# Kernel tuning notes

Measured on AMD Instinct MI355X. Metric: run time of the kernel, lower is better.

Reference implementation:

```python
import jax, jax.numpy as jnp
import numpy as np

S, N, H, AD, AR = 256, 1024, 512, 128, 2

def setup_inputs() -> dict:
    key = jax.random.key(0)
    k0, k1, k2, k3, k4, k5 = jax.random.split(key, 6)
    xav1 = np.sqrt(2.0 / (H + AD)).astype(np.float32)   # xavier_normal std for [H,AD]
    xav2 = np.sqrt(2.0 / (AD + AR)).astype(np.float32)  # xavier_normal std for [AD,AR]
    return {
        "pre_emb_padded": jax.random.normal(k0, (S, N, H), jnp.float32),
        "fol_emb_padded": jax.random.normal(k1, (S, N, H), jnp.float32),
        "pre_attn_mask": jnp.zeros((N, S), jnp.bool_),
        "fol_attn_mask": jnp.zeros((N, S), jnp.bool_),
        "pre_is_valid": jnp.ones((N,), jnp.int32),
        "fol_is_valid": jnp.ones((N,), jnp.int32),
        "W1_pre": jax.random.normal(k2, (H, AD), jnp.float32) * xav1,
        "W2_pre": jax.random.normal(k3, (AD, AR), jnp.float32) * xav2,
        "W1_fol": jax.random.normal(k4, (H, AD), jnp.float32) * xav1,
        "W2_fol": jax.random.normal(k5, (AD, AR), jnp.float32) * xav2,
    }

def _attn_pool(emb, mask, W1, W2):
    # emb: [S, N, H] -> x: [N, S, H]
    x = jnp.transpose(emb, (1, 0, 2))
    s = jnp.tanh(x @ W1) @ W2                 # [N, S, 2]
    s = jax.nn.softmax(s, axis=1)             # softmax over seq (first softmax)
    s = jnp.transpose(s, (0, 2, 1))           # [N, 2, S]
    s = jnp.where(mask[:, None, :], -jnp.inf, s)
    s = jax.nn.softmax(s, axis=-1)            # masked second softmax over seq
    return jnp.einsum('nrs,nsh->nrh', s, x)   # [N, 2, H]

def _scatter_valid(h, valid):
    # reproduce the python valid-list gather: valid rows take next chunk, else zeros
    pos = jnp.cumsum(valid) - 1               # [N]
    return jnp.where((valid > 0)[:, None, None], h[pos], jnp.zeros((), h.dtype))

def reference(pre_emb_padded, fol_emb_padded, pre_attn_mask, fol_attn_mask,
              pre_is_valid, fol_is_valid, W1_pre, W2_pre, W1_fol, W2_fol):
    h_pre = _scatter_valid(_attn_pool(pre_emb_padded, pre_attn_mask, W1_pre, W2_pre), pre_is_valid)
    h_fol = _scatter_valid(_attn_pool(fol_emb_padded, fol_attn_mask, W1_fol, W2_fol), fol_is_valid)
    # mean over the attn_r=2 rows, concat along feature dim -> [N, 1, 2H]
    return jnp.concatenate([h_pre.mean(axis=1, keepdims=True),
                            h_fol.mean(axis=1, keepdims=True)], axis=2)
```

## Files before the change

kernel.cpp:

```cpp
#include <hip/hip_runtime.h>
#include <hip/hip_bf16.h>
#include <cstdint>
#include <cstddef>

#define S_ 256
#define N_ 1024
#define H_ 512
#define AD_ 128
static constexpr int M_TOTAL = N_ * S_;

typedef __attribute__((ext_vector_type(8))) short short8;
typedef __attribute__((ext_vector_type(4))) float f32x4;

#define LDS_BARRIER()                                       \
  asm volatile("s_waitcnt lgkmcnt(0)" ::: "memory");        \
  __builtin_amdgcn_s_barrier()

__device__ __forceinline__ float red16_dpp(float v) {
  union fi { float f; int i; };
  fi a, r;
  a.f = v;
  r.i = __builtin_amdgcn_update_dpp(0, a.i, 0xB1, 0xF, 0xF, true);
  a.f += r.f;
  r.i = __builtin_amdgcn_update_dpp(0, a.i, 0x4E, 0xF, 0xF, true);
  a.f += r.f;
  r.i = __builtin_amdgcn_update_dpp(0, a.i, 0x124, 0xF, 0xF, true);
  a.f += r.f;
  r.i = __builtin_amdgcn_update_dpp(0, a.i, 0x128, 0xF, 0xF, true);
  a.f += r.f;
  return a.f;
}

__global__ __launch_bounds__(256) void k_w1frag(
    const float* __restrict__ w1_pre, const float* __restrict__ w1_fol,
    unsigned short* __restrict__ w1f) {
  int idx = blockIdx.x * 256 + threadIdx.x;
  int st = blockIdx.y;
  const float* w1 = st ? w1_fol : w1_pre;
  int j = idx & 7;
  int lane = (idx >> 3) & 63;
  int c = (idx >> 9) & 7;
  int kk = idx >> 12;
  int k = kk * 32 + ((lane >> 4) << 3) + j;
  int d = c * 16 + (lane & 15);
  __hip_bfloat16 hb = __float2bfloat16(w1[(size_t)k * AD_ + d]);
  w1f[(size_t)st * 65536 + idx] = *(unsigned short*)&hb;
}

__global__ __launch_bounds__(1024) void k_scan(
    const int* __restrict__ valid_pre, const int* __restrict__ valid_fol,
    int* __restrict__ pos) {
  const int st = blockIdx.x;
  const int* valid = st ? valid_fol : valid_pre;
  __shared__ int buf[1024];
  const int t = threadIdx.x;
  buf[t] = valid[t];
  __syncthreads();
  for (int off = 1; off < 1024; off <<= 1) {
    int v = (t >= off) ? buf[t - off] : 0;
    __syncthreads();
    buf[t] += v;
    __syncthreads();
  }
  pos[st * N_ + t] = buf[t] - 1;
}

__global__ __launch_bounds__(512) void k_logits(
    const float* __restrict__ emb_pre, const float* __restrict__ emb_fol,
    const unsigned short* __restrict__ w1f,
    const float* __restrict__ w2_pre, const float* __restrict__ w2_fol,
    float* __restrict__ logits) {
  __shared__ __align__(16) unsigned char As[32768];
  __shared__ float part[2][8][16][2];

  const int bid = blockIdx.x;
  const int st  = bid >> 7;
  const int idx = bid & 127;
  const int nc  = idx >> 1;
  const int sh  = idx & 1;
  const int n0 = nc * 16, s0 = sh * 128;
  const float* __restrict__ emb = st ? emb_fol : emb_pre;
  const float* __restrict__ w2  = st ? w2_fol : w2_pre;

  const int t = threadIdx.x;
  const int w = t >> 6, lane = t & 63;
  const int r16 = lane & 15, kq = lane >> 4;

  short8 B[16];
  {
    const unsigned short* bb = w1f + (size_t)st * 65536 + w * 512 + (size_t)lane * 8;
#pragma unroll
    for (int kk = 0; kk < 16; ++kk) B[kk] = *(const short8*)(bb + kk * 4096);
  }
  const float w2v0 = w2[(w * 16 + r16) * 2 + 0];
  const float w2v1 = w2[(w * 16 + r16) * 2 + 1];

  const int srow = t >> 5;
  const int sl   = t & 31;
  const size_t SSTR = (size_t)N_ * H_;
  const float* sbase = emb + ((size_t)s0 * N_ + n0 + srow) * H_ + sl * 4;
  unsigned wadr[4];
#pragma unroll
  for (int j = 0; j < 4; ++j) {
    int g = j * 16 + (sl >> 1);
    wadr[j] = (unsigned)(srow * 1024 + ((g ^ (srow & 7)) * 16) + (sl & 1) * 8);
  }
  const int rrow = w * 2 + ((lane >> 1) & 1);
  const int rr   = lane & 1;

  float4 nxt[4];
#pragma unroll
  for (int j = 0; j < 4; ++j) nxt[j] = *(const float4*)(sbase + j * 128);
#pragma unroll
  for (int j = 0; j < 4; ++j) {
    union { unsigned long long u; __hip_bfloat162 h[2]; } p;
    p.h[0] = __float22bfloat162_rn(make_float2(nxt[j].x, nxt[j].y));
    p.h[1] = __float22bfloat162_rn(make_float2(nxt[j].z, nxt[j].w));
    *(unsigned long long*)&As[wadr[j]] = p.u;
  }
#pragma unroll
  for (int j = 0; j < 4; ++j) nxt[j] = *(const float4*)(sbase + SSTR + j * 128);
  LDS_BARRIER();

  for (int ss = 0; ss < 128; ++ss) {
    const int cur = ss & 1;
    const int nb  = cur ^ 1;
    const unsigned abase = (unsigned)(cur << 14);

    if (ss < 127) {
#pragma unroll
      for (int j = 0; j < 4; ++j) {
        union { unsigned long long u; __hip_bfloat162 h[2]; } p;
        p.h[0] = __float22bfloat162_rn(make_float2(nxt[j].x, nxt[j].y));
        p.h[1] = __float22bfloat162_rn(make_float2(nxt[j].z, nxt[j].w));
        *(unsigned long long*)&As[(nb << 14) + wadr[j]] = p.u;
      }
    }
    if (ss < 126) {
      const float* nbp = sbase + (size_t)(ss + 2) * SSTR;
#pragma unroll
      for (int j = 0; j < 4; ++j) nxt[j] = *(const float4*)(nbp + j * 128);
    }
    if (ss > 0 && lane < 4) {
      float v = 0.f;
#pragma unroll
      for (int g = 0; g < 8; ++g) v += part[nb][g][rrow][rr];
      logits[((size_t)st * M_TOTAL + (size_t)(s0 + ss - 1) * N_ + n0 + rrow) * 2 + rr] = v;
    }

    f32x4 acc0 = (f32x4){0.f, 0.f, 0.f, 0.f};
    f32x4 acc1 = (f32x4){0.f, 0.f, 0.f, 0.f};
#pragma unroll
    for (int kk = 0; kk < 16; ++kk) {
      const unsigned ra = abase +
          (unsigned)(r16 * 1024 + (((kk * 4 + kq) ^ (r16 & 7)) * 16));
      short8 a = *(const short8*)&As[ra];
      if (kk & 1)
        acc1 = __builtin_amdgcn_mfma_f32_16x16x32_bf16(a, B[kk], acc1, 0, 0, 0);
      else
        acc0 = __builtin_amdgcn_mfma_f32_16x16x32_bf16(a, B[kk], acc0, 0, 0, 0);
    }

#pragma unroll
    for (int q = 0; q < 4; ++q) {
      float xc = fminf(fmaxf(acc0[q] + acc1[q], -10.f), 10.f);
      float e  = __expf(2.f * xc);
      float th = (e - 1.f) / (e + 1.f);
      float p0 = red16_dpp(th * w2v0);
      float p1 = red16_dpp(th * w2v1);
      if (r16 == 0) {
        part[cur][w][kq * 4 + q][0] = p0;
        part[cur][w][kq * 4 + q][1] = p1;
      }
    }
    LDS_BARRIER();
  }

  if (lane < 4) {
    float v = 0.f;
#pragma unroll
    for (int g = 0; g < 8; ++g) v += part[1][g][rrow][rr];
    logits[((size_t)st * M_TOTAL + (size_t)(s0 + 127) * N_ + n0 + rrow) * 2 + rr] = v;
  }
}

template <bool MAXRED>
__device__ __forceinline__ float blockRed(float v, float* buf) {
#pragma unroll
  for (int off = 32; off; off >>= 1) {
    float o = __shfl_xor(v, off);
    v = MAXRED ? fmaxf(v, o) : (v + o);
  }
  __syncthreads();
  if ((threadIdx.x & 63) == 0) buf[threadIdx.x >> 6] = v;
  __syncthreads();
  float r = buf[0];
#pragma unroll
  for (int i = 1; i < 4; ++i) r = MAXRED ? fmaxf(r, buf[i]) : (r + buf[i]);
  return r;
}

__global__ __launch_bounds__(256) void k_softmax(
    const float* __restrict__ logits,
    const unsigned char* __restrict__ mask_pre, const unsigned char* __restrict__ mask_fol,
    float* __restrict__ wbar) {
  const int n  = blockIdx.x;
  const int st = blockIdx.y;
  const unsigned char* mask = st ? mask_fol : mask_pre;
  const int s = threadIdx.x;

  float2 l = *(const float2*)&logits[((size_t)st * M_TOTAL + (size_t)s * N_ + n) * 2];
  const bool mk = mask[(size_t)n * S_ + s] != 0;

  __shared__ float buf[4];
  float q[2];
  float lv[2] = {l.x, l.y};
#pragma unroll
  for (int r = 0; r < 2; ++r) {
    float m1 = blockRed<true>(lv[r], buf);
    float e1 = __expf(lv[r] - m1);
    float s1 = blockRed<false>(e1, buf);
    float p1 = e1 / s1;
    float v  = mk ? -INFINITY : p1;
    float m2 = blockRed<true>(v, buf);
    float e2 = mk ? 0.f : __expf(v - m2);
    float s2 = blockRed<false>(e2, buf);
    q[r] = e2 / s2;
  }
  wbar[((size_t)st * N_ + n) * S_ + s] = 0.5f * (q[0] + q[1]);
}

__global__ __launch_bounds__(512) void k_pv2(
    const float* __restrict__ emb_pre, const float* __restrict__ emb_fol,
    const float* __restrict__ wbar,
    float* __restrict__ part) {
  const int bid = blockIdx.x;
  const int st  = bid >> 7;
  const int idx = bid & 127;
  const int nc  = idx >> 1;
  const int sh  = idx & 1;
  const int n0 = nc * 16, s0 = sh * 128;
  const float* __restrict__ emb = st ? emb_fol : emb_pre;

  const int t = threadIdx.x;
  const int nl = t >> 5;
  const int c0 = (t & 31) * 4;

  __shared__ float wl[16][128];
  for (int i = t; i < 2048; i += 512) {
    int j = i >> 7, sl = i & 127;
    wl[j][sl] = wbar[((size_t)st * N_ + n0 + j) * S_ + s0 + sl];
  }
  __syncthreads();

  float4 acc[4], cur[4], nxt[4];
#pragma unroll
  for (int j = 0; j < 4; ++j) acc[j] = (float4){0.f, 0.f, 0.f, 0.f};

  const float* rowp = emb + ((size_t)(s0 + 127) * N_ + n0 + nl) * H_ + c0;
  const size_t SSTR = (size_t)N_ * H_;
#pragma unroll
  for (int j = 0; j < 4; ++j) cur[j] = *(const float4*)(rowp + j * 128);

  for (int sl = 127; sl >= 0; --sl) {
    const float* nrow = rowp - SSTR;
    if (sl > 0) {
#pragma unroll
      for (int j = 0; j < 4; ++j) nxt[j] = *(const float4*)(nrow + j * 128);
    }
    const float wv = wl[nl][sl];
#pragma unroll
    for (int j = 0; j < 4; ++j) {
      acc[j].x += wv * cur[j].x;
      acc[j].y += wv * cur[j].y;
      acc[j].z += wv * cur[j].z;
      acc[j].w += wv * cur[j].w;
    }
#pragma unroll
    for (int j = 0; j < 4; ++j) cur[j] = nxt[j];
    rowp = nrow;
  }

  float* pp = part + (((size_t)(st * 2 + sh) * N_) + n0 + nl) * H_ + c0;
#pragma unroll
  for (int j = 0; j < 4; ++j) *(float4*)(pp + j * 128) = acc[j];
}

__global__ __launch_bounds__(256) void k_combine(
    const float* __restrict__ part, const int* __restrict__ pos,
    const int* __restrict__ valid_pre, const int* __restrict__ valid_fol,
    float* __restrict__ out) {
  const int n = blockIdx.x, t = threadIdx.x;
  const int st = t >> 7;
  const int c = (t & 127) * 4;
  const int* valid = st ? valid_fol : valid_pre;
  float4 r = {0.f, 0.f, 0.f, 0.f};
  if (valid[n] > 0) {
    int np = pos[st * N_ + n]; if (np < 0) np = 0;
    float4 a = *(const float4*)&part[(((size_t)(st * 2 + 0) * N_) + np) * H_ + c];
    float4 b = *(const float4*)&part[(((size_t)(st * 2 + 1) * N_) + np) * H_ + c];
    r.x = a.x + b.x; r.y = a.y + b.y; r.z = a.z + b.z; r.w = a.w + b.w;
  }
  *(float4*)&out[(size_t)n * 1024 + st * 512 + c] = r;
}

extern "C" void kernel_launch(void* const* d_in, const int* in_sizes, int n_in,
                              void* d_out, int out_size, void* d_ws, size_t ws_size,
                              hipStream_t stream) {
  const float* emb_pre = (const float*)d_in[0];
  const float* emb_fol = (const float*)d_in[1];
  const unsigned char* mask_pre = (const unsigned char*)d_in[2];
  const unsigned char* mask_fol = (const unsigned char*)d_in[3];
  const int* valid_pre = (const int*)d_in[4];
  const int* valid_fol = (const int*)d_in[5];
  const float* w1_pre = (const float*)d_in[6];
  const float* w2_pre = (const float*)d_in[7];
  const float* w1_fol = (const float*)d_in[8];
  const float* w2_fol = (const float*)d_in[9];
  float* out = (float*)d_out;

  char* ws = (char*)d_ws;
  unsigned short* w1f = (unsigned short*)ws;
  int*   pos    = (int*)(ws + 262144);
  float* logits = (float*)(ws + 270336);
  float* wbar   = (float*)(ws + 270336 + 4194304);
  float* part   = (float*)(ws + 270336 + 4194304 + 2097152);

  hipLaunchKernelGGL(k_w1frag, dim3(256, 2), dim3(256), 0, stream,
                     w1_pre, w1_fol, w1f);
  hipLaunchKernelGGL(k_scan, dim3(2), dim3(1024), 0, stream,
                     valid_pre, valid_fol, pos);
  hipLaunchKernelGGL(k_logits, dim3(256), dim3(512), 0, stream,
                     emb_pre, emb_fol, w1f, w2_pre, w2_fol, logits);
  hipLaunchKernelGGL(k_softmax, dim3(N_, 2), dim3(256), 0, stream,
                     logits, mask_pre, mask_fol, wbar);
  hipLaunchKernelGGL(k_pv2, dim3(256), dim3(512), 0, stream,
                     emb_pre, emb_fol, wbar, part);
  hipLaunchKernelGGL(k_combine, dim3(N_), dim3(256), 0, stream,
                     part, pos, valid_pre, valid_fol, out);
}
```

Measured before the change: 399.4 us.

## Fuse softmax into PV kernel and process two seq steps per logits iteration

The separate softmax kernel is removed. Each PV block now recomputes the double softmax for its 16 rows over all 256 positions from the logits, using warp shuffles, and keeps the weights in LDS. This drops one launch and the wbar round trip through global memory, at the cost of each of the two s-halves repeating the softmax work. The logits kernel also now stages two sequence positions per iteration with 64KB of LDS and runs twice as many MFMAs per barrier, which halves the barrier count but may reduce occupancy.

```diff
diff --git a/kernel.cpp b/kernel.cpp
--- a/kernel.cpp
+++ b/kernel.cpp
@@ -70,8 +70,8 @@
     const unsigned short* __restrict__ w1f,
     const float* __restrict__ w2_pre, const float* __restrict__ w2_fol,
     float* __restrict__ logits) {
-  __shared__ __align__(16) unsigned char As[32768];
-  __shared__ float part[2][8][16][2];
+  __shared__ __align__(16) unsigned char As[65536];
+  __shared__ float part[2][8][2][16][2];
 
   const int bid = blockIdx.x;
   const int st  = bid >> 7;
@@ -95,144 +95,108 @@
   const float w2v0 = w2[(w * 16 + r16) * 2 + 0];
   const float w2v1 = w2[(w * 16 + r16) * 2 + 1];
 
-  const int srow = t >> 5;
-  const int sl   = t & 31;
+  const int srow = t >> 4, sl = t & 15;
+  const int s_local = srow >> 4, nrow = srow & 15;
   const size_t SSTR = (size_t)N_ * H_;
-  const float* sbase = emb + ((size_t)s0 * N_ + n0 + srow) * H_ + sl * 4;
-  unsigned wadr[4];
-#pragma unroll
-  for (int j = 0; j < 4; ++j) {
-    int g = j * 16 + (sl >> 1);
+  const float* sbase = emb + ((size_t)(s0 + s_local) * N_ + n0 + nrow) * H_ + sl * 4;
+  unsigned wadr[8];
+#pragma unroll
+  for (int j = 0; j < 8; ++j) {
+    int g = j * 8 + (sl >> 1);
     wadr[j] = (unsigned)(srow * 1024 + ((g ^ (srow & 7)) * 16) + (sl & 1) * 8);
   }
-  const int rrow = w * 2 + ((lane >> 1) & 1);
-  const int rr   = lane & 1;
-
-  float4 nxt[4];
-#pragma unroll
-  for (int j = 0; j < 4; ++j) nxt[j] = *(const float4*)(sbase + j * 128);
-#pragma unroll
-  for (int j = 0; j < 4; ++j) {
+  const int vv = w * 8 + lane;
+  const int drg = vv >> 5, dn = (vv >> 1) & 15, drr = vv & 1;
+
+  float4 nxt[8];
+#pragma unroll
+  for (int j = 0; j < 8; ++j) nxt[j] = *(const float4*)(sbase + j * 64);
+#pragma unroll
+  for (int j = 0; j < 8; ++j) {
     union { unsigned long long u; __hip_bfloat162 h[2]; } p;
     p.h[0] = __float22bfloat162_rn(make_float2(nxt[j].x, nxt[j].y));
     p.h[1] = __float22bfloat162_rn(make_float2(nxt[j].z, nxt[j].w));
     *(unsigned long long*)&As[wadr[j]] = p.u;
   }
 #pragma unroll
-  for (int j = 0; j < 4; ++j) nxt[j] = *(const float4*)(sbase + SSTR + j * 128);
+  for (int j = 0; j < 8; ++j) nxt[j] = *(const float4*)(sbase + 2 * SSTR + j * 64);
   LDS_BARRIER();
 
-  for (int ss = 0; ss < 128; ++ss) {
+  for (int ss = 0; ss < 64; ++ss) {
     const int cur = ss & 1;
     const int nb  = cur ^ 1;
-    const unsigned abase = (unsigned)(cur << 14);
-
-    if (ss < 127) {
-#pragma unroll
-      for (int j = 0; j < 4; ++j) {
+    const unsigned abase = (unsigned)(cur << 15);
+
+    if (ss < 63) {
+#pragma unroll
+      for (int j = 0; j < 8; ++j) {
         union { unsigned long long u; __hip_bfloat162 h[2]; } p;
         p.h[0] = __float22bfloat162_rn(make_float2(nxt[j].x, nxt[j].y));
         p.h[1] = __float22bfloat162_rn(make_float2(nxt[j].z, nxt[j].w));
-        *(unsigned long long*)&As[(nb << 14) + wadr[j]] = p.u;
+        *(unsigned long long*)&As[(nb << 15) + wadr[j]] = p.u;
       }
     }
-    if (ss < 126) {
-      const float* nbp = sbase + (size_t)(ss + 2) * SSTR;
-#pragma unroll
-      for (int j = 0; j < 4; ++j) nxt[j] = *(const float4*)(nbp + j * 128);
-    }
-    if (ss > 0 && lane < 4) {
+    if (ss < 62) {
+      const float* nbp = sbase + (size_t)(2 * (ss + 2)) * SSTR;
+#pragma unroll
+      for (int j = 0; j < 8; ++j) nxt[j] = *(const float4*)(nbp + j * 64);
+    }
+    if (ss > 0 && lane < 8) {
       float v = 0.f;
 #pragma unroll
-      for (int g = 0; g < 8; ++g) v += part[nb][g][rrow][rr];
-      logits[((size_t)st * M_TOTAL + (size_t)(s0 + ss - 1) * N_ + n0 + rrow) * 2 + rr] = v;
-    }
-
-    f32x4 acc0 = (f32x4){0.f, 0.f, 0.f, 0.f};
-    f32x4 acc1 = (f32x4){0.f, 0.f, 0.f, 0.f};
+      for (int g = 0; g < 8; ++g) v += part[nb][g][drg][dn][drr];
+      int s_out = s0 + 2 * (ss - 1) + drg;
+      logits[((size_t)st * M_TOTAL + (size_t)s_out * N_ + n0 + dn) * 2 + drr] = v;
+    }
+
+    f32x4 a00 = (f32x4){0.f, 0.f, 0.f, 0.f}, a01 = a00, a10 = a00, a11 = a00;
 #pragma unroll
     for (int kk = 0; kk < 16; ++kk) {
-      const unsigned ra = abase +
+      const unsigned ra0 = abase +
           (unsigned)(r16 * 1024 + (((kk * 4 + kq) ^ (r16 & 7)) * 16));
-      short8 a = *(const short8*)&As[ra];
-      if (kk & 1)
-        acc1 = __builtin_amdgcn_mfma_f32_16x16x32_bf16(a, B[kk], acc1, 0, 0, 0);
-      else
-        acc0 = __builtin_amdgcn_mfma_f32_16x16x32_bf16(a, B[kk], acc0, 0, 0, 0);
-    }
-
-#pragma unroll
-    for (int q = 0; q < 4; ++q) {
-      float xc = fminf(fmaxf(acc0[q] + acc1[q], -10.f), 10.f);
-      float e  = __expf(2.f * xc);
-      float th = (e - 1.f) / (e + 1.f);
-      float p0 = red16_dpp(th * w2v0);
-      float p1 = red16_dpp(th * w2v1);
-      if (r16 == 0) {
-        part[cur][w][kq * 4 + q][0] = p0;
-        part[cur][w][kq * 4 + q][1] = p1;
+      short8 f0 = *(const short8*)&As[ra0];
+      short8 f1 = *(const short8*)&As[ra0 + 16384];
+      if (kk & 1) {
+        a01 = __builtin_amdgcn_mfma_f32_16x16x32_bf16(f0, B[kk], a01, 0, 0, 0);
+        a11 = __builtin_amdgcn_mfma_f32_16x16x32_bf16(f1, B[kk], a11, 0, 0, 0);
+      } else {
+        a00 = __builtin_amdgcn_mfma_f32_16x16x32_bf16(f0, B[kk], a00, 0, 0, 0);
+        a10 = __builtin_amdgcn_mfma_f32_16x16x32_bf16(f1, B[kk], a10, 0, 0, 0);
       }
     }
+
+#pragma unroll
+    for (int rg = 0; rg < 2; ++rg) {
+#pragma unroll
+      for (int q = 0; q < 4; ++q) {
+        float av = rg ? (a10[q] + a11[q]) : (a00[q] + a01[q]);
+        float xc = fminf(fmaxf(av, -10.f), 10.f);
+        float e  = __expf(2.f * xc);
+        float th = (e - 1.f) / (e + 1.f);
+        float p0 = red16_dpp(th * w2v0);
+        float p1 = red16_dpp(th * w2v1);
+        if (r16 == 0) {
+          part[cur][w][rg][kq * 4 + q][0] = p0;
+          part[cur][w][rg][kq * 4 + q][1] = p1;
+        }
+      }
+    }
     LDS_BARRIER();
   }
 
-  if (lane < 4) {
+  if (lane < 8) {
     float v = 0.f;
 #pragma unroll
-    for (int g = 0; g < 8; ++g) v += part[1][g][rrow][rr];
-    logits[((size_t)st * M_TOTAL + (size_t)(s0 + 127) * N_ + n0 + rrow) * 2 + rr] = v;
-  }
-}
-
-template <bool MAXRED>
-__device__ __forceinline__ float blockRed(float v, float* buf) {
-#pragma unroll
-  for (int off = 32; off; off >>= 1) {
-    float o = __shfl_xor(v, off);
-    v = MAXRED ? fmaxf(v, o) : (v + o);
-  }
-  __syncthreads();
-  if ((threadIdx.x & 63) == 0) buf[threadIdx.x >> 6] = v;
-  __syncthreads();
-  float r = buf[0];
-#pragma unroll
-  for (int i = 1; i < 4; ++i) r = MAXRED ? fmaxf(r, buf[i]) : (r + buf[i]);
-  return r;
-}
-
-__global__ __launch_bounds__(256) void k_softmax(
+    for (int g = 0; g < 8; ++g) v += part[1][g][drg][dn][drr];
+    int s_out = s0 + 126 + drg;
+    logits[((size_t)st * M_TOTAL + (size_t)s_out * N_ + n0 + dn) * 2 + drr] = v;
+  }
+}
+
+__global__ __launch_bounds__(512) void k_pv2(
+    const float* __restrict__ emb_pre, const float* __restrict__ emb_fol,
     const float* __restrict__ logits,
     const unsigned char* __restrict__ mask_pre, const unsigned char* __restrict__ mask_fol,
-    float* __restrict__ wbar) {
-  const int n  = blockIdx.x;
-  const int st = blockIdx.y;
-  const unsigned char* mask = st ? mask_fol : mask_pre;
-  const int s = threadIdx.x;
-
-  float2 l = *(const float2*)&logits[((size_t)st * M_TOTAL + (size_t)s * N_ + n) * 2];
-  const bool mk = mask[(size_t)n * S_ + s] != 0;
-
-  __shared__ float buf[4];
-  float q[2];
-  float lv[2] = {l.x, l.y};
-#pragma unroll
-  for (int r = 0; r < 2; ++r) {
-    float m1 = blockRed<true>(lv[r], buf);
-    float e1 = __expf(lv[r] - m1);
-    float s1 = blockRed<false>(e1, buf);
-    float p1 = e1 / s1;
-    float v  = mk ? -INFINITY : p1;
-    float m2 = blockRed<true>(v, buf);
-    float e2 = mk ? 0.f : __expf(v - m2);
-    float s2 = blockRed<false>(e2, buf);
-    q[r] = e2 / s2;
-  }
-  wbar[((size_t)st * N_ + n) * S_ + s] = 0.5f * (q[0] + q[1]);
-}
-
-__global__ __launch_bounds__(512) void k_pv2(
-    const float* __restrict__ emb_pre, const float* __restrict__ emb_fol,
-    const float* __restrict__ wbar,
     float* __restrict__ part) {
   const int bid = blockIdx.x;
   const int st  = bid >> 7;
@@ -241,17 +205,68 @@
   const int sh  = idx & 1;
   const int n0 = nc * 16, s0 = sh * 128;
   const float* __restrict__ emb = st ? emb_fol : emb_pre;
+  const unsigned char* __restrict__ mask = st ? mask_fol : mask_pre;
 
   const int t = threadIdx.x;
+  __shared__ float wl[16][S_];
+
+  {
+    const int nn = t >> 5;
+    const int g  = t & 31;
+    const int n  = n0 + nn;
+    float l0[8], l1[8];
+    bool mk[8];
+#pragma unroll
+    for (int i = 0; i < 8; ++i) {
+      int s = g * 8 + i;
+      float2 l = *(const float2*)&logits[((size_t)st * M_TOTAL + (size_t)s * N_ + n) * 2];
+      l0[i] = l.x;
+      l1[i] = l.y;
+      mk[i] = mask[(size_t)n * S_ + s] != 0;
+    }
+    float q0[8], q1[8];
+#pragma unroll
+    for (int r = 0; r < 2; ++r) {
+      float* lv = r ? l1 : l0;
+      float* qq = r ? q1 : q0;
+      float m1 = lv[0];
+#pragma unroll
+      for (int i = 1; i < 8; ++i) m1 = fmaxf(m1, lv[i]);
+#pragma unroll
+      for (int off = 16; off; off >>= 1) m1 = fmaxf(m1, __shfl_xor(m1, off));
+      float e[8], s1 = 0.f;
+#pragma unroll
+      for (int i = 0; i < 8; ++i) { e[i] = __expf(lv[i] - m1); s1 += e[i]; }
+#pragma unroll
+      for (int off = 16; off; off >>= 1) s1 += __shfl_xor(s1, off);
+      float inv1 = 1.f / s1;
+      float v[8];
+#pragma unroll
+      for (int i = 0; i < 8; ++i) v[i] = mk[i] ? -INFINITY : e[i] * inv1;
+      float m2 = v[0];
+#pragma unroll
+      for (int i = 1; i < 8; ++i) m2 = fmaxf(m2, v[i]);
+#pragma unroll
+      for (int off = 16; off; off >>= 1) m2 = fmaxf(m2, __shfl_xor(m2, off));
+      float e2[8], s2 = 0.f;
+#pragma unroll
+      for (int i = 0; i < 8; ++i) {
+        e2[i] = mk[i] ? 0.f : __expf(v[i] - m2);
+        s2 += e2[i];
+      }
+#pragma unroll
+      for (int off = 16; off; off >>= 1) s2 += __shfl_xor(s2, off);
+      float inv2 = 1.f / s2;
+#pragma unroll
+      for (int i = 0; i < 8; ++i) qq[i] = e2[i] * inv2;
+    }
+#pragma unroll
+    for (int i = 0; i < 8; ++i) wl[nn][g * 8 + i] = 0.5f * (q0[i] + q1[i]);
+  }
+  __syncthreads();
+
   const int nl = t >> 5;
   const int c0 = (t & 31) * 4;
-
-  __shared__ float wl[16][128];
-  for (int i = t; i < 2048; i += 512) {
-    int j = i >> 7, sl = i & 127;
-    wl[j][sl] = wbar[((size_t)st * N_ + n0 + j) * S_ + s0 + sl];
-  }
-  __syncthreads();
 
   float4 acc[4], cur[4], nxt[4];
 #pragma unroll
@@ -268,7 +283,7 @@
 #pragma unroll
       for (int j = 0; j < 4; ++j) nxt[j] = *(const float4*)(nrow + j * 128);
     }
-    const float wv = wl[nl][sl];
+    const float wv = wl[nl][s0 + sl];
 #pragma unroll
     for (int j = 0; j < 4; ++j) {
       acc[j].x += wv * cur[j].x;
@@ -323,8 +338,7 @@
   unsigned short* w1f = (unsigned short*)ws;
   int*   pos    = (int*)(ws + 262144);
   float* logits = (float*)(ws + 270336);
-  float* wbar   = (float*)(ws + 270336 + 4194304);
-  float* part   = (float*)(ws + 270336 + 4194304 + 2097152);
+  float* part   = (float*)(ws + 270336 + 4194304);
 
   hipLaunchKernelGGL(k_w1frag, dim3(256, 2), dim3(256), 0, stream,
                      w1_pre, w1_fol, w1f);
@@ -332,10 +346,8 @@
                      valid_pre, valid_fol, pos);
   hipLaunchKernelGGL(k_logits, dim3(256), dim3(512), 0, stream,
                      emb_pre, emb_fol, w1f, w2_pre, w2_fol, logits);
-  hipLaunchKernelGGL(k_softmax, dim3(N_, 2), dim3(256), 0, stream,
-                     logits, mask_pre, mask_fol, wbar);
   hipLaunchKernelGGL(k_pv2, dim3(256), dim3(512), 0, stream,
-                     emb_pre, emb_fol, wbar, part);
+                     emb_pre, emb_fol, logits, mask_pre, mask_fol, part);
   hipLaunchKernelGGL(k_combine, dim3(N_), dim3(256), 0, stream,
                      part, pos, valid_pre, valid_fol, out);
 }
```

Result: faster. 372.5 us (median of 2 runs) (-6.7%).

## Fuse logits, double softmax and weighted pooling into one per-row kernel

Applied to the files above, without the earlier changes.

Replaces the separate logits, softmax and pooling kernels with a single kernel that handles one (stream, n) row per block. Each block computes all 256 logits with MFMA, runs both softmaxes in one wavefront from LDS, and then re-reads the same row's embeddings for pooling while they may still be cached. This removes the logits and wbar global round trips and the two-way split-S partials, and it aims to cut the second full HBM pass over the embeddings. In exchange there are more, smaller blocks with short MFMA loops and serialized phases. A dummy LDS pad array is added to cap occupancy, which could also limit latency hiding.

```diff
diff --git a/kernel.cpp b/kernel.cpp
--- a/kernel.cpp
+++ b/kernel.cpp
@@ -65,24 +65,29 @@
   pos[st * N_ + t] = buf[t] - 1;
 }
 
-__global__ __launch_bounds__(512) void k_logits(
+__global__ __launch_bounds__(512) void k_fused(
     const float* __restrict__ emb_pre, const float* __restrict__ emb_fol,
     const unsigned short* __restrict__ w1f,
     const float* __restrict__ w2_pre, const float* __restrict__ w2_fol,
-    float* __restrict__ logits) {
+    const unsigned char* __restrict__ mask_pre, const unsigned char* __restrict__ mask_fol,
+    float* __restrict__ part) {
   __shared__ __align__(16) unsigned char As[32768];
-  __shared__ float part[2][8][16][2];
+  __shared__ float partb[2][8][16][2];
+  __shared__ float lgbuf[S_][2];
+  __shared__ float wl[S_];
+  __shared__ __align__(16) float p3[4][128][4];
+  __shared__ float pad_[9216];
+
+  const int t = threadIdx.x;
+  if (blockDim.y == 2) pad_[t] = 0.f;
 
   const int bid = blockIdx.x;
-  const int st  = bid >> 7;
-  const int idx = bid & 127;
-  const int nc  = idx >> 1;
-  const int sh  = idx & 1;
-  const int n0 = nc * 16, s0 = sh * 128;
+  const int st  = bid >> 10;
+  const int n   = bid & 1023;
   const float* __restrict__ emb = st ? emb_fol : emb_pre;
   const float* __restrict__ w2  = st ? w2_fol : w2_pre;
-
-  const int t = threadIdx.x;
+  const unsigned char* __restrict__ mask = st ? mask_fol : mask_pre;
+
   const int w = t >> 6, lane = t & 63;
   const int r16 = lane & 15, kq = lane >> 4;
 
@@ -95,195 +100,173 @@
   const float w2v0 = w2[(w * 16 + r16) * 2 + 0];
   const float w2v1 = w2[(w * 16 + r16) * 2 + 1];
 
-  const int srow = t >> 5;
-  const int sl   = t & 31;
   const size_t SSTR = (size_t)N_ * H_;
-  const float* sbase = emb + ((size_t)s0 * N_ + n0 + srow) * H_ + sl * 4;
+  const float* baseA = emb + ((size_t)w * N_ + n) * H_;
   unsigned wadr[4];
 #pragma unroll
   for (int j = 0; j < 4; ++j) {
-    int g = j * 16 + (sl >> 1);
-    wadr[j] = (unsigned)(srow * 1024 + ((g ^ (srow & 7)) * 16) + (sl & 1) * 8);
-  }
-  const int rrow = w * 2 + ((lane >> 1) & 1);
-  const int rr   = lane & 1;
+    int cb = (j & 1) * 1024 + lane * 16;
+    int R  = (j >> 1) * 8 + w;
+    int g16 = cb >> 5, half = (cb >> 4) & 1;
+    wadr[j] = (unsigned)(R * 1024 + ((g16 ^ (R & 7)) * 16) + half * 8);
+  }
 
   float4 nxt[4];
-#pragma unroll
-  for (int j = 0; j < 4; ++j) nxt[j] = *(const float4*)(sbase + j * 128);
-#pragma unroll
-  for (int j = 0; j < 4; ++j) {
-    union { unsigned long long u; __hip_bfloat162 h[2]; } p;
-    p.h[0] = __float22bfloat162_rn(make_float2(nxt[j].x, nxt[j].y));
-    p.h[1] = __float22bfloat162_rn(make_float2(nxt[j].z, nxt[j].w));
-    *(unsigned long long*)&As[wadr[j]] = p.u;
-  }
-#pragma unroll
-  for (int j = 0; j < 4; ++j) nxt[j] = *(const float4*)(sbase + SSTR + j * 128);
+#define LD_STEP(MS)                                                          \
+  {                                                                          \
+    _Pragma("unroll")                                                        \
+    for (int j = 0; j < 4; ++j)                                              \
+      nxt[j] = *(const float4*)(baseA + (size_t)(MS) * 16 * SSTR +           \
+                                (size_t)(j >> 1) * 8 * SSTR +                \
+                                (j & 1) * 256 + lane * 4);                   \
+  }
+#define ST_STEP(BUFB)                                                        \
+  {                                                                          \
+    _Pragma("unroll")                                                        \
+    for (int j = 0; j < 4; ++j) {                                            \
+      union { unsigned long long u; __hip_bfloat162 h[2]; } p;               \
+      p.h[0] = __float22bfloat162_rn(make_float2(nxt[j].x, nxt[j].y));       \
+      p.h[1] = __float22bfloat162_rn(make_float2(nxt[j].z, nxt[j].w));       \
+      *(unsigned long long*)&As[(BUFB) + wadr[j]] = p.u;                     \
+    }                                                                        \
+  }
+
+  LD_STEP(0);
+  ST_STEP(0);
+  LD_STEP(1);
   LDS_BARRIER();
 
-  for (int ss = 0; ss < 128; ++ss) {
+  for (int ss = 0; ss < 16; ++ss) {
     const int cur = ss & 1;
     const int nb  = cur ^ 1;
     const unsigned abase = (unsigned)(cur << 14);
 
-    if (ss < 127) {
-#pragma unroll
-      for (int j = 0; j < 4; ++j) {
-        union { unsigned long long u; __hip_bfloat162 h[2]; } p;
-        p.h[0] = __float22bfloat162_rn(make_float2(nxt[j].x, nxt[j].y));
-        p.h[1] = __float22bfloat162_rn(make_float2(nxt[j].z, nxt[j].w));
-        *(unsigned long long*)&As[(nb << 14) + wadr[j]] = p.u;
-      }
-    }
-    if (ss < 126) {
-      const float* nbp = sbase + (size_t)(ss + 2) * SSTR;
-#pragma unroll
-      for (int j = 0; j < 4; ++j) nxt[j] = *(const float4*)(nbp + j * 128);
-    }
+    if (ss < 15) ST_STEP((unsigned)(nb << 14));
+    if (ss < 14) LD_STEP(ss + 2);
+
     if (ss > 0 && lane < 4) {
+      int vv = w * 4 + lane;
+      int row = vv >> 1, rr = vv & 1;
       float v = 0.f;
 #pragma unroll
-      for (int g = 0; g < 8; ++g) v += part[nb][g][rrow][rr];
-      logits[((size_t)st * M_TOTAL + (size_t)(s0 + ss - 1) * N_ + n0 + rrow) * 2 + rr] = v;
-    }
-
-    f32x4 acc0 = (f32x4){0.f, 0.f, 0.f, 0.f};
-    f32x4 acc1 = (f32x4){0.f, 0.f, 0.f, 0.f};
+      for (int g = 0; g < 8; ++g) v += partb[nb][g][row][rr];
+      lgbuf[(ss - 1) * 16 + row][rr] = v;
+    }
+
+    f32x4 a0 = (f32x4){0.f, 0.f, 0.f, 0.f};
+    f32x4 a1 = (f32x4){0.f, 0.f, 0.f, 0.f};
 #pragma unroll
     for (int kk = 0; kk < 16; ++kk) {
       const unsigned ra = abase +
           (unsigned)(r16 * 1024 + (((kk * 4 + kq) ^ (r16 & 7)) * 16));
       short8 a = *(const short8*)&As[ra];
       if (kk & 1)
-        acc1 = __builtin_amdgcn_mfma_f32_16x16x32_bf16(a, B[kk], acc1, 0, 0, 0);
+        a1 = __builtin_amdgcn_mfma_f32_16x16x32_bf16(a, B[kk], a1, 0, 0, 0);
       else
-        acc0 = __builtin_amdgcn_mfma_f32_16x16x32_bf16(a, B[kk], acc0, 0, 0, 0);
+        a0 = __builtin_amdgcn_mfma_f32_16x16x32_bf16(a, B[kk], a0, 0, 0, 0);
     }
 
 #pragma unroll
     for (int q = 0; q < 4; ++q) {
-      float xc = fminf(fmaxf(acc0[q] + acc1[q], -10.f), 10.f);
+      float xc = fminf(fmaxf(a0[q] + a1[q], -10.f), 10.f);
       float e  = __expf(2.f * xc);
       float th = (e - 1.f) / (e + 1.f);
       float p0 = red16_dpp(th * w2v0);
       float p1 = red16_dpp(th * w2v1);
       if (r16 == 0) {
-        part[cur][w][kq * 4 + q][0] = p0;
-        part[cur][w][kq * 4 + q][1] = p1;
+        partb[cur][w][kq * 4 + q][0] = p0;
+        partb[cur][w][kq * 4 + q][1] = p1;
       }
     }
     LDS_BARRIER();
   }
 
   if (lane < 4) {
+    int vv = w * 4 + lane;
+    int row = vv >> 1, rr = vv & 1;
     float v = 0.f;
 #pragma unroll
-    for (int g = 0; g < 8; ++g) v += part[1][g][rrow][rr];
-    logits[((size_t)st * M_TOTAL + (size_t)(s0 + 127) * N_ + n0 + rrow) * 2 + rr] = v;
-  }
-}
-
-template <bool MAXRED>
-__device__ __forceinline__ float blockRed(float v, float* buf) {
-#pragma unroll
-  for (int off = 32; off; off >>= 1) {
-    float o = __shfl_xor(v, off);
-    v = MAXRED ? fmaxf(v, o) : (v + o);
-  }
-  __syncthreads();
-  if ((threadIdx.x & 63) == 0) buf[threadIdx.x >> 6] = v;
-  __syncthreads();
-  float r = buf[0];
-#pragma unroll
-  for (int i = 1; i < 4; ++i) r = MAXRED ? fmaxf(r, buf[i]) : (r + buf[i]);
-  return r;
-}
-
-__global__ __launch_bounds__(256) void k_softmax(
-    const float* __restrict__ logits,
-    const unsigned char* __restrict__ mask_pre, const unsigned char* __restrict__ mask_fol,
-    float* __restrict__ wbar) {
-  const int n  = blockIdx.x;
-  const int st = blockIdx.y;
-  const unsigned char* mask = st ? mask_fol : mask_pre;
-  const int s = threadIdx.x;
-
-  float2 l = *(const float2*)&logits[((size_t)st * M_TOTAL + (size_t)s * N_ + n) * 2];
-  const bool mk = mask[(size_t)n * S_ + s] != 0;
-
-  __shared__ float buf[4];
-  float q[2];
-  float lv[2] = {l.x, l.y};
-#pragma unroll
-  for (int r = 0; r < 2; ++r) {
-    float m1 = blockRed<true>(lv[r], buf);
-    float e1 = __expf(lv[r] - m1);
-    float s1 = blockRed<false>(e1, buf);
-    float p1 = e1 / s1;
-    float v  = mk ? -INFINITY : p1;
-    float m2 = blockRed<true>(v, buf);
-    float e2 = mk ? 0.f : __expf(v - m2);
-    float s2 = blockRed<false>(e2, buf);
-    q[r] = e2 / s2;
-  }
-  wbar[((size_t)st * N_ + n) * S_ + s] = 0.5f * (q[0] + q[1]);
-}
-
-__global__ __launch_bounds__(512) void k_pv2(
-    const float* __restrict__ emb_pre, const float* __restrict__ emb_fol,
-    const float* __restrict__ wbar,
-    float* __restrict__ part) {
-  const int bid = blockIdx.x;
-  const int st  = bid >> 7;
-  const int idx = bid & 127;
-  const int nc  = idx >> 1;
-  const int sh  = idx & 1;
-  const int n0 = nc * 16, s0 = sh * 128;
-  const float* __restrict__ emb = st ? emb_fol : emb_pre;
-
-  const int t = threadIdx.x;
-  const int nl = t >> 5;
-  const int c0 = (t & 31) * 4;
-
-  __shared__ float wl[16][128];
-  for (int i = t; i < 2048; i += 512) {
-    int j = i >> 7, sl = i & 127;
-    wl[j][sl] = wbar[((size_t)st * N_ + n0 + j) * S_ + s0 + sl];
-  }
-  __syncthreads();
-
-  float4 acc[4], cur[4], nxt[4];
-#pragma unroll
-  for (int j = 0; j < 4; ++j) acc[j] = (float4){0.f, 0.f, 0.f, 0.f};
-
-  const float* rowp = emb + ((size_t)(s0 + 127) * N_ + n0 + nl) * H_ + c0;
-  const size_t SSTR = (size_t)N_ * H_;
-#pragma unroll
-  for (int j = 0; j < 4; ++j) cur[j] = *(const float4*)(rowp + j * 128);
-
-  for (int sl = 127; sl >= 0; --sl) {
-    const float* nrow = rowp - SSTR;
-    if (sl > 0) {
-#pragma unroll
-      for (int j = 0; j < 4; ++j) nxt[j] = *(const float4*)(nrow + j * 128);
-    }
-    const float wv = wl[nl][sl];
-#pragma unroll
-    for (int j = 0; j < 4; ++j) {
-      acc[j].x += wv * cur[j].x;
-      acc[j].y += wv * cur[j].y;
-      acc[j].z += wv * cur[j].z;
-      acc[j].w += wv * cur[j].w;
-    }
-#pragma unroll
-    for (int j = 0; j < 4; ++j) cur[j] = nxt[j];
-    rowp = nrow;
-  }
-
-  float* pp = part + (((size_t)(st * 2 + sh) * N_) + n0 + nl) * H_ + c0;
-#pragma unroll
-  for (int j = 0; j < 4; ++j) *(float4*)(pp + j * 128) = acc[j];
+    for (int g = 0; g < 8; ++g) v += partb[1][g][row][rr];
+    lgbuf[240 + row][rr] = v;
+  }
+  LDS_BARRIER();
+
+  if (w == 0) {
+    uchar4 mkb = *(const uchar4*)(mask + (size_t)n * S_ + lane * 4);
+    float l0[4], l1[4];
+    bool mk[4];
+#pragma unroll
+    for (int i = 0; i < 4; ++i) {
+      l0[i] = lgbuf[lane * 4 + i][0];
+      l1[i] = lgbuf[lane * 4 + i][1];
+    }
+    mk[0] = mkb.x != 0; mk[1] = mkb.y != 0; mk[2] = mkb.z != 0; mk[3] = mkb.w != 0;
+    float q0[4], q1[4];
+#pragma unroll
+    for (int r = 0; r < 2; ++r) {
+      float* lv = r ? l1 : l0;
+      float* qq = r ? q1 : q0;
+      float m1 = fmaxf(fmaxf(lv[0], lv[1]), fmaxf(lv[2], lv[3]));
+#pragma unroll
+      for (int off = 32; off; off >>= 1) m1 = fmaxf(m1, __shfl_xor(m1, off));
+      float e[4], s1 = 0.f;
+#pragma unroll
+      for (int i = 0; i < 4; ++i) { e[i] = __expf(lv[i] - m1); s1 += e[i]; }
+#pragma unroll
+      for (int off = 32; off; off >>= 1) s1 += __shfl_xor(s1, off);
+      float inv1 = 1.f / s1;
+      float v[4];
+#pragma unroll
+      for (int i = 0; i < 4; ++i) v[i] = mk[i] ? -INFINITY : e[i] * inv1;
+      float m2 = fmaxf(fmaxf(v[0], v[1]), fmaxf(v[2], v[3]));
+#pragma unroll
+      for (int off = 32; off; off >>= 1) m2 = fmaxf(m2, __shfl_xor(m2, off));
+      float e2[4], s2 = 0.f;
+#pragma unroll
+      for (int i = 0; i < 4; ++i) { e2[i] = mk[i] ? 0.f : __expf(v[i] - m2); s2 += e2[i]; }
+#pragma unroll
+      for (int off = 32; off; off >>= 1) s2 += __shfl_xor(s2, off);
+      float inv2 = 1.f / s2;
+#pragma unroll
+      for (int i = 0; i < 4; ++i) qq[i] = e2[i] * inv2;
+    }
+#pragma unroll
+    for (int i = 0; i < 4; ++i) wl[lane * 4 + i] = 0.5f * (q0[i] + q1[i]);
+  }
+  LDS_BARRIER();
+
+  {
+    const int sg = t >> 7, tt = t & 127, c0 = tt * 4;
+    const float* embn = emb + (size_t)n * H_ + c0;
+    float4 acc = (float4){0.f, 0.f, 0.f, 0.f};
+    const int sTop = sg * 64 + 63;
+#pragma unroll
+    for (int b2 = 0; b2 < 8; ++b2) {
+      const int sb = sTop - b2 * 8;
+      float4 x[8];
+#pragma unroll
+      for (int i = 0; i < 8; ++i)
+        x[i] = *(const float4*)(embn + (size_t)(sb - i) * SSTR);
+#pragma unroll
+      for (int i = 0; i < 8; ++i) {
+        const float wv = wl[sb - i];
+        acc.x += wv * x[i].x;
+        acc.y += wv * x[i].y;
+        acc.z += wv * x[i].z;
+        acc.w += wv * x[i].w;
+      }
+    }
+    *(float4*)&p3[sg][tt][0] = acc;
+  }
+  LDS_BARRIER();
+  if (t < 128) {
+    float4 r;
+    r.x = p3[0][t][0] + p3[1][t][0] + p3[2][t][0] + p3[3][t][0];
+    r.y = p3[0][t][1] + p3[1][t][1] + p3[2][t][1] + p3[3][t][1];
+    r.z = p3[0][t][2] + p3[1][t][2] + p3[2][t][2] + p3[3][t][2];
+    r.w = p3[0][t][3] + p3[1][t][3] + p3[2][t][3] + p3[3][t][3];
+    *(float4*)&part[((size_t)st * N_ + n) * H_ + t * 4] = r;
+  }
 }
 
 __global__ __launch_bounds__(256) void k_combine(
@@ -297,9 +280,7 @@
   float4 r = {0.f, 0.f, 0.f, 0.f};
   if (valid[n] > 0) {
     int np = pos[st * N_ + n]; if (np < 0) np = 0;
-    float4 a = *(const float4*)&part[(((size_t)(st * 2 + 0) * N_) + np) * H_ + c];
-    float4 b = *(const float4*)&part[(((size_t)(st * 2 + 1) * N_) + np) * H_ + c];
-    r.x = a.x + b.x; r.y = a.y + b.y; r.z = a.z + b.z; r.w = a.w + b.w;
+    r = *(const float4*)&part[((size_t)st * N_ + np) * H_ + c];
   }
   *(float4*)&out[(size_t)n * 1024 + st * 512 + c] = r;
 }
@@ -322,20 +303,15 @@
   char* ws = (char*)d_ws;
   unsigned short* w1f = (unsigned short*)ws;
   int*   pos    = (int*)(ws + 262144);
-  float* logits = (float*)(ws + 270336);
-  float* wbar   = (float*)(ws + 270336 + 4194304);
-  float* part   = (float*)(ws + 270336 + 4194304 + 2097152);
+  float* part   = (float*)(ws + 270336);
 
   hipLaunchKernelGGL(k_w1frag, dim3(256, 2), dim3(256), 0, stream,
                      w1_pre, w1_fol, w1f);
   hipLaunchKernelGGL(k_scan, dim3(2), dim3(1024), 0, stream,
                      valid_pre, valid_fol, pos);
-  hipLaunchKernelGGL(k_logits, dim3(256), dim3(512), 0, stream,
-                     emb_pre, emb_fol, w1f, w2_pre, w2_fol, logits);
-  hipLaunchKernelGGL(k_softmax, dim3(N_, 2), dim3(256), 0, stream,
-                     logits, mask_pre, mask_fol, wbar);
-  hipLaunchKernelGGL(k_pv2, dim3(256), dim3(512), 0, stream,
-                     emb_pre, emb_fol, wbar, part);
+  hipLaunchKernelGGL(k_fused, dim3(2048), dim3(512), 0, stream,
+                     emb_pre, emb_fol, w1f, w2_pre, w2_fol,
+                     mask_pre, mask_fol, part);
   hipLaunchKernelGGL(k_combine, dim3(N_), dim3(256), 0, stream,
                      part, pos, valid_pre, valid_fol, out);
 }
```

Result: faster. 383.9 us (-3.9%).
